# Kernel optimization log

Hardware: AMD Instinct MI355X
Metric: run time of the kernel (lower is better)

## Reference

```python
import jax, jax.numpy as jnp
import numpy as np

N_NODES = 100000
N_EDGES = 1600000
D = 128  # in_feats = n_hidden = out_feats


def _linear_params(key, d_in, d_out):
    kw, kb = jax.random.split(key)
    scale = 1.0 / np.sqrt(d_in)
    W = jax.random.uniform(kw, (d_in, d_out), jnp.float32, -scale, scale)
    b = jax.random.uniform(kb, (d_out,), jnp.float32, -scale, scale)
    return W, b


def setup_inputs() -> dict:
    key = jax.random.key(0)
    keys = jax.random.split(key, 8)
    x = jax.random.normal(keys[0], (N_NODES, D), jnp.float32)
    edge_index = jax.random.randint(keys[1], (2, N_EDGES), 0, N_NODES, jnp.int64)
    inp = {"x": x, "edge_index": edge_index}
    for l in range(3):
        W1, b1 = _linear_params(keys[2 + 2 * l], D, D)
        W2, b2 = _linear_params(keys[3 + 2 * l], D, D)
        inp[f"W1_{l}"] = W1
        inp[f"b1_{l}"] = b1
        inp[f"W2_{l}"] = W2
        inp[f"b2_{l}"] = b2
    return inp


def _gin_conv(x, src, dst, W1, b1, W2, b2):
    # GINConv: MLP((1+eps)*x + sum_{j->i} x_j), eps=0
    agg = jax.ops.segment_sum(x[src], dst, num_segments=N_NODES)
    h = agg + x
    h = jnp.maximum(h @ W1 + b1, 0.0)
    return h @ W2 + b2


def reference(x, edge_index, W1_0, b1_0, W2_0, b2_0,
              W1_1, b1_1, W2_1, b2_1, W1_2, b1_2, W2_2, b2_2):
    src, dst = edge_index[0], edge_index[1]
    # layer 0 (loop body): conv -> relu
    x = jnp.maximum(_gin_conv(x, src, dst, W1_0, b1_0, W2_0, b2_0), 0.0)
    # layer 1 (num_layers-2): conv -> relu -> dropout (eval: identity)
    x = jnp.maximum(_gin_conv(x, src, dst, W1_1, b1_1, W2_1, b2_1), 0.0)
    # layer 2 (last): conv -> relu
    x = jnp.maximum(_gin_conv(x, src, dst, W1_2, b1_2, W2_2, b2_2), 0.0)
    return x
```

## Files before the change

kernel.cpp:

```cpp
#include <hip/hip_runtime.h>

#define N_NODES 100000
#define N_EDGES 1600000
#define D 128
#define NBUCK 98
#define CAP 20480

typedef __attribute__((ext_vector_type(8))) short bf16x8;
typedef __attribute__((ext_vector_type(4))) float f32x4;
typedef unsigned long long u64;

__device__ __forceinline__ float b2f_lo(unsigned int u) {
    return __builtin_bit_cast(float, u << 16);
}
__device__ __forceinline__ float b2f_hi(unsigned int u) {
    return __builtin_bit_cast(float, u & 0xFFFF0000u);
}
__device__ __forceinline__ unsigned short f2b(float f) {
    unsigned int u = __builtin_bit_cast(unsigned int, f);
    u += 0x7FFFu + ((u >> 16) & 1u);
    return (unsigned short)(u >> 16);
}


__global__ __launch_bounds__(256) void prep_kernel(
    const float* __restrict__ x, unsigned short* __restrict__ xb,
    const float* __restrict__ W0, const float* __restrict__ W1_, const float* __restrict__ W2_,
    const float* __restrict__ W3, const float* __restrict__ W4, const float* __restrict__ W5,
    unsigned short* __restrict__ T0, unsigned short* __restrict__ T1_,
    unsigned short* __restrict__ T2_, unsigned short* __restrict__ T3,
    unsigned short* __restrict__ T4, unsigned short* __restrict__ T5,
    uint4* __restrict__ dob4, uint4* __restrict__ xbs4) {
    int blk = blockIdx.x;
    if (blk < 384) {
        const float* W;
        unsigned short* T;
        switch (blk >> 6) {
            case 0: W = W0; T = T0; break;
            case 1: W = W1_; T = T1_; break;
            case 2: W = W2_; T = T2_; break;
            case 3: W = W3; T = T3; break;
            case 4: W = W4; T = T4; break;
            default: W = W5; T = T5; break;
        }
        int i = (blk & 63) * 256 + threadIdx.x;
        int k = i >> 7, n = i & 127;
        T[n * 128 + k] = f2b(W[i]);
    } else if (blk < 12884) {
        int i = (blk - 384) * 256 + threadIdx.x;
        if (i < 3200000) {
            float4 v = ((const float4*)x)[i];
            ushort4 o;
            o.x = f2b(v.x); o.y = f2b(v.y); o.z = f2b(v.z); o.w = f2b(v.w);
            ((ushort4*)xb)[i] = o;
        }
    } else {
        int i = (blk - 12884) * 256 + threadIdx.x;
        uint4 z = {0u, 0u, 0u, 0u};
        if (i < 256) dob4[i] = z;
        if (i < 16) xbs4[i] = z;
    }
}


__global__ __launch_bounds__(256) void bin_kernel(const int* __restrict__ src,
                                                  const int* __restrict__ dst,
                                                  int* __restrict__ bcur,
                                                  u64* __restrict__ ebuf) {
    __shared__ int h[NBUCK];
    __shared__ int base[NBUCK];
    int tid = threadIdx.x;
    if (tid < NBUCK) h[tid] = 0;
    __syncthreads();
    int e0 = blockIdx.x * 2048;
    int myd[8], mys[8];
#pragma unroll
    for (int i = 0; i < 8; i++) {
        int e = e0 + tid + i * 256;
        int dv = (e < N_EDGES) ? dst[e] : -1;
        myd[i] = dv;
        mys[i] = (e < N_EDGES) ? src[e] : 0;
        if (dv >= 0) atomicAdd(&h[dv >> 10], 1);
    }
    __syncthreads();
    if (tid < NBUCK) {
        int c = h[tid];
        base[tid] = (c > 0) ? (tid * CAP + atomicAdd(&bcur[tid], c)) : 0;
        h[tid] = 0;
    }
    __syncthreads();
#pragma unroll
    for (int i = 0; i < 8; i++) {
        int dv = myd[i];
        if (dv >= 0) {
            int b = dv >> 10;
            int p = base[b] + atomicAdd(&h[b], 1);
            if (p < (b + 1) * CAP)
                ebuf[p] = ((u64)(unsigned int)dv << 32) | (unsigned int)mys[i];
        }
    }
}

__global__ __launch_bounds__(1024) void bucket_hist_kernel(const u64* __restrict__ ebuf,
                                                           const int* __restrict__ bcur,
                                                           int* __restrict__ deg,
                                                           int* __restrict__ ptot) {
    __shared__ int hist[1024];
    int b = blockIdx.x, tid = threadIdx.x;
    int nE = bcur[b]; if (nE > CAP) nE = CAP;
    const u64* slab = ebuf + (size_t)b * CAP;
    hist[tid] = 0;
    __syncthreads();
    for (int i = tid; i < nE; i += 1024)
        atomicAdd(&hist[(int)(slab[i] >> 32) & 1023], 1);
    __syncthreads();
    int node = b * 1024 + tid;
    int d = hist[tid];
    if (node < N_NODES) deg[node] = d;
    int dp = (node < N_NODES) ? ((d + 3) & ~3) : 0;
    __syncthreads();
    hist[tid] = dp;
    __syncthreads();
#pragma unroll
    for (int s = 512; s > 0; s >>= 1) {
        if (tid < s) hist[tid] += hist[tid + s];
        __syncthreads();
    }
    if (tid == 0) ptot[b] = hist[0];
}

__global__ __launch_bounds__(128) void pscan_kernel(const int* __restrict__ ptot,
                                                    int* __restrict__ bbase,
                                                    int* __restrict__ off) {
    __shared__ int s[128];
    int tid = threadIdx.x;
    int v = (tid < NBUCK) ? ptot[tid] : 0;
    s[tid] = v;
    __syncthreads();
#pragma unroll
    for (int d = 1; d < 128; d <<= 1) {
        int t = (tid >= d) ? s[tid - d] : 0;
        __syncthreads();
        s[tid] += t;
        __syncthreads();
    }
    if (tid < NBUCK) bbase[tid] = s[tid] - v;
    if (tid == 127) off[N_NODES] = s[127];
}

__global__ __launch_bounds__(1024) void bucket_csr_kernel(const u64* __restrict__ ebuf,
                                                          const int* __restrict__ bcur,
                                                          const int* __restrict__ deg,
                                                          const int* __restrict__ bbase,
                                                          int* __restrict__ off,
                                                          int* __restrict__ csr) {
    __shared__ int sc[1024];
    __shared__ int cnt[1024];
    int b = blockIdx.x, tid = threadIdx.x;
    int nE = bcur[b]; if (nE > CAP) nE = CAP;
    int base = bbase[b];
    const u64* slab = ebuf + (size_t)b * CAP;
    int node = b * 1024 + tid;
    int d = (node < N_NODES) ? deg[node] : 0;
    int dp = (node < N_NODES) ? ((d + 3) & ~3) : 0;
    sc[tid] = dp;
    cnt[tid] = 0;
    __syncthreads();
#pragma unroll
    for (int s = 1; s < 1024; s <<= 1) {
        int t = (tid >= s) ? sc[tid - s] : 0;
        __syncthreads();
        sc[tid] += t;
        __syncthreads();
    }
    int excl = sc[tid] - dp;
    sc[tid] = excl;
    if (node < N_NODES) off[node] = base + excl;
    __syncthreads();
    for (int i = tid; i < nE; i += 1024) {
        u64 e = slab[i];
        int dd = (int)(e >> 32) & 1023;
        int pos = sc[dd] + atomicAdd(&cnt[dd], 1);
        csr[base + pos] = (int)(e & 0xFFFFFFFFu);
    }
    for (int j = d; j < dp; j++) csr[base + excl + j] = N_NODES;
}


__global__ __launch_bounds__(256) void agg_bf16(const uint4* __restrict__ xb4,
                                                const int* __restrict__ off,
                                                const int* __restrict__ csr,
                                                uint4* __restrict__ t4) {
    int node = blockIdx.x * 4 + (threadIdx.x >> 6);
    if (node >= N_NODES) return;
    int lane = threadIdx.x & 63;
    int g = lane >> 4;
    int c = lane & 15;
    uint4 me = xb4[(size_t)node * 16 + c];
    float w0 = (g == 0) ? 1.0f : 0.0f;
    float a0 = b2f_lo(me.x) * w0, a1 = b2f_hi(me.x) * w0;
    float a2 = b2f_lo(me.y) * w0, a3 = b2f_hi(me.y) * w0;
    float a4 = b2f_lo(me.z) * w0, a5 = b2f_hi(me.z) * w0;
    float a6 = b2f_lo(me.w) * w0, a7 = b2f_hi(me.w) * w0;
    int k = off[node], e = off[node + 1];
#define PICK4(q) ((g & 2) ? ((g & 1) ? (q).w : (q).z) : ((g & 1) ? (q).y : (q).x))
#define ACC8(v) { a0 += b2f_lo((v).x); a1 += b2f_hi((v).x); \
                  a2 += b2f_lo((v).y); a3 += b2f_hi((v).y); \
                  a4 += b2f_lo((v).z); a5 += b2f_hi((v).z); \
                  a6 += b2f_lo((v).w); a7 += b2f_hi((v).w); }
    for (; k + 16 <= e; k += 16) {
        int4 q0 = *(const int4*)(csr + k);
        int4 q1 = *(const int4*)(csr + k + 4);
        int4 q2 = *(const int4*)(csr + k + 8);
        int4 q3 = *(const int4*)(csr + k + 12);
        int n0 = PICK4(q0), n1 = PICK4(q1), n2 = PICK4(q2), n3 = PICK4(q3);
        uint4 v0 = xb4[(size_t)n0 * 16 + c];
        uint4 v1 = xb4[(size_t)n1 * 16 + c];
        uint4 v2 = xb4[(size_t)n2 * 16 + c];
        uint4 v3 = xb4[(size_t)n3 * 16 + c];
        ACC8(v0); ACC8(v1); ACC8(v2); ACC8(v3);
    }
    for (; k < e; k += 4) {
        int4 q = *(const int4*)(csr + k);
        int n = PICK4(q);
        uint4 v = xb4[(size_t)n * 16 + c];
        ACC8(v);
    }
#undef PICK4
#undef ACC8
    a0 += __shfl_xor(a0, 16); a1 += __shfl_xor(a1, 16);
    a2 += __shfl_xor(a2, 16); a3 += __shfl_xor(a3, 16);
    a4 += __shfl_xor(a4, 16); a5 += __shfl_xor(a5, 16);
    a6 += __shfl_xor(a6, 16); a7 += __shfl_xor(a7, 16);
    a0 += __shfl_xor(a0, 32); a1 += __shfl_xor(a1, 32);
    a2 += __shfl_xor(a2, 32); a3 += __shfl_xor(a3, 32);
    a4 += __shfl_xor(a4, 32); a5 += __shfl_xor(a5, 32);
    a6 += __shfl_xor(a6, 32); a7 += __shfl_xor(a7, 32);
    if (g == 0) {
        uint4 o;
        o.x = (unsigned int)f2b(a0) | ((unsigned int)f2b(a1) << 16);
        o.y = (unsigned int)f2b(a2) | ((unsigned int)f2b(a3) << 16);
        o.z = (unsigned int)f2b(a4) | ((unsigned int)f2b(a5) << 16);
        o.w = (unsigned int)f2b(a6) | ((unsigned int)f2b(a7) << 16);
        t4[(size_t)node * 16 + c] = o;
    }
}


template <bool OUT_F32>
__global__ __launch_bounds__(256) void mlp_mfma(const unsigned short* __restrict__ A,
                                                const unsigned short* __restrict__ W1t,
                                                const float* __restrict__ bias1,
                                                const unsigned short* __restrict__ W2t,
                                                const float* __restrict__ bias2,
                                                void* __restrict__ out) {
    __shared__ char smem[4 * 8704];
    int tid = threadIdx.x;
    int wave = tid >> 6, lane = tid & 63;
    int quad = lane >> 4, mr = lane & 15;
    int m_base = blockIdx.x * 128 + wave * 32;
    int m0 = m_base + mr;       if (m0 >= N_NODES) m0 = N_NODES - 1;
    int m1 = m_base + 16 + mr;  if (m1 >= N_NODES) m1 = N_NODES - 1;

    unsigned short* ust = (unsigned short*)(smem + wave * 8704);

    bf16x8 a0[4], a1[4];
#pragma unroll
    for (int kc = 0; kc < 4; kc++) {
        a0[kc] = *(const bf16x8*)(A + (size_t)m0 * D + kc * 32 + quad * 8);
        a1[kc] = *(const bf16x8*)(A + (size_t)m1 * D + kc * 32 + quad * 8);
    }

    f32x4 acc0[8], acc1[8];
#pragma unroll
    for (int nt = 0; nt < 8; nt++) { acc0[nt] = (f32x4)0.0f; acc1[nt] = (f32x4)0.0f; }
#pragma unroll
    for (int nt = 0; nt < 8; nt++) {
        const unsigned short* wp = W1t + (size_t)(nt * 16 + mr) * D + quad * 8;
#pragma unroll
        for (int kc = 0; kc < 4; kc++) {
            bf16x8 b = *(const bf16x8*)(wp + kc * 32);
            acc0[nt] = __builtin_amdgcn_mfma_f32_16x16x32_bf16(a0[kc], b, acc0[nt], 0, 0, 0);
            acc1[nt] = __builtin_amdgcn_mfma_f32_16x16x32_bf16(a1[kc], b, acc1[nt], 0, 0, 0);
        }
    }
#pragma unroll
    for (int nt = 0; nt < 8; nt++) {
        float bv = bias1[nt * 16 + mr];
#pragma unroll
        for (int r = 0; r < 4; r++) {
            ust[(quad * 4 + r) * 136 + nt * 16 + mr] = f2b(fmaxf(acc0[nt][r] + bv, 0.0f));
            ust[2176 + (quad * 4 + r) * 136 + nt * 16 + mr] = f2b(fmaxf(acc1[nt][r] + bv, 0.0f));
        }
    }

#pragma unroll
    for (int kc = 0; kc < 4; kc++) {
        a0[kc] = *(const bf16x8*)&ust[mr * 136 + kc * 32 + quad * 8];
        a1[kc] = *(const bf16x8*)&ust[2176 + mr * 136 + kc * 32 + quad * 8];
    }
#pragma unroll
    for (int nt = 0; nt < 8; nt++) { acc0[nt] = (f32x4)0.0f; acc1[nt] = (f32x4)0.0f; }
#pragma unroll
    for (int nt = 0; nt < 8; nt++) {
        const unsigned short* wp = W2t + (size_t)(nt * 16 + mr) * D + quad * 8;
#pragma unroll
        for (int kc = 0; kc < 4; kc++) {
            bf16x8 b = *(const bf16x8*)(wp + kc * 32);
            acc0[nt] = __builtin_amdgcn_mfma_f32_16x16x32_bf16(a0[kc], b, acc0[nt], 0, 0, 0);
            acc1[nt] = __builtin_amdgcn_mfma_f32_16x16x32_bf16(a1[kc], b, acc1[nt], 0, 0, 0);
        }
    }

    if (OUT_F32) {
        float* st = (float*)ust;
        const int S = 132;
        float* op = (float*)out;
#pragma unroll
        for (int s = 0; s < 2; s++) {
#pragma unroll
            for (int nt = 0; nt < 8; nt++) {
                float bv = bias2[nt * 16 + mr];
#pragma unroll
                for (int r = 0; r < 4; r++) {
                    float v = s ? acc1[nt][r] : acc0[nt][r];
                    st[(quad * 4 + r) * S + nt * 16 + mr] = fmaxf(v + bv, 0.0f);
                }
            }
#pragma unroll
            for (int it = 0; it < 8; it++) {
                int linear = lane + it * 64;
                int row = linear >> 5, col = (linear & 31) << 2;
                int gm = m_base + s * 16 + row;
                if (gm < N_NODES) {
                    float4 val = *(float4*)&st[row * S + col];
                    *(float4*)(op + (size_t)gm * D + col) = val;
                }
            }
        }
    } else {
        const int S = 136;
        unsigned short* op = (unsigned short*)out;
#pragma unroll
        for (int s = 0; s < 2; s++) {
            unsigned short* st = ust + s * 2176;
#pragma unroll
            for (int nt = 0; nt < 8; nt++) {
                float bv = bias2[nt * 16 + mr];
#pragma unroll
                for (int r = 0; r < 4; r++) {
                    float v = s ? acc1[nt][r] : acc0[nt][r];
                    st[(quad * 4 + r) * S + nt * 16 + mr] = f2b(fmaxf(v + bv, 0.0f));
                }
            }
#pragma unroll
            for (int it = 0; it < 4; it++) {
                int linear = lane + it * 64;
                int row = linear >> 4, col = (linear & 15) << 3;
                int gm = m_base + s * 16 + row;
                if (gm < N_NODES) {
                    uint4 val = *(uint4*)&st[row * S + col];
                    *(uint4*)(op + (size_t)gm * D + col) = val;
                }
            }
        }
    }
}


extern "C" void kernel_launch(void* const* d_in, const int* in_sizes, int n_in,
                              void* d_out, int out_size, void* d_ws, size_t ws_size,
                              hipStream_t stream) {
    const float* x = (const float*)d_in[0];
    const int* ei = (const int*)d_in[1];
    const int* srcv = ei;
    const int* dstv = ei + N_EDGES;
    const float* W1[3] = {(const float*)d_in[2], (const float*)d_in[6], (const float*)d_in[10]};
    const float* b1[3] = {(const float*)d_in[3], (const float*)d_in[7], (const float*)d_in[11]};
    const float* W2[3] = {(const float*)d_in[4], (const float*)d_in[8], (const float*)d_in[12]};
    const float* b2[3] = {(const float*)d_in[5], (const float*)d_in[9], (const float*)d_in[13]};

    char* ws = (char*)d_ws;
    int* off = (int*)ws;
    unsigned short* Wt[6];
    for (int i = 0; i < 6; i++) Wt[i] = (unsigned short*)(ws + 401408 + i * 32768);
    int* csr = (int*)(ws + 598016);
    unsigned short* xb = (unsigned short*)(ws + 8198144);
    unsigned short* P  = (unsigned short*)(ws + 33798400);

    char* dob = (char*)d_out;
    int* bcur  = (int*)(dob);
    int* deg   = (int*)(dob + 4096);
    int* ptot  = (int*)(dob + 450560);
    int* bbase = (int*)(dob + 454656);
    u64* ebuf  = (u64*)(dob + 1048576);

    prep_kernel<<<12885, 256, 0, stream>>>(
        x, xb,
        W1[0], W2[0], W1[1], W2[1], W1[2], W2[2],
        Wt[0], Wt[1], Wt[2], Wt[3], Wt[4], Wt[5],
        (uint4*)dob, (uint4*)(xb + (size_t)N_NODES * D));

    bin_kernel<<<782, 256, 0, stream>>>(srcv, dstv, bcur, ebuf);
    bucket_hist_kernel<<<NBUCK, 1024, 0, stream>>>(ebuf, bcur, deg, ptot);
    pscan_kernel<<<1, 128, 0, stream>>>(ptot, bbase, off);
    bucket_csr_kernel<<<NBUCK, 1024, 0, stream>>>(ebuf, bcur, deg, bbase, off, csr);

    const int agg_grid = 25000;
    const int mlp_grid = (N_NODES + 127) / 128;

    agg_bf16<<<agg_grid, 256, 0, stream>>>((const uint4*)xb, off, csr, (uint4*)P);
    mlp_mfma<false><<<mlp_grid, 256, 0, stream>>>(P, Wt[0], b1[0], Wt[1], b2[0], xb);
    agg_bf16<<<agg_grid, 256, 0, stream>>>((const uint4*)xb, off, csr, (uint4*)P);
    mlp_mfma<false><<<mlp_grid, 256, 0, stream>>>(P, Wt[2], b1[1], Wt[3], b2[1], xb);
    agg_bf16<<<agg_grid, 256, 0, stream>>>((const uint4*)xb, off, csr, (uint4*)P);
    mlp_mfma<true><<<mlp_grid, 256, 0, stream>>>(P, Wt[4], b1[2], Wt[5], b2[2], d_out);
}
```

Baseline: 504.9 us.

## Split bf16 features into 8 column-group planes for cache-resident gather aggregation

Stores node features as 8 column-group planes of 16 bf16 values each (32 bytes per node per plane). The aggregation kernel gives each block a single column group, so the gathered working set per plane (~3.2 MB) can stay in cache, with 8 lanes per node and edge indices shuffled across lanes. CSR padding goes from multiples of 4 to multiples of 8, and the CSR array moves into the output buffer. The MLP loads and stores are adapted to the planar layout, at the cost of 32-byte gather granularity and more padded edges.

```diff
diff --git a/kernel.cpp b/kernel.cpp
--- a/kernel.cpp
+++ b/kernel.cpp
@@ -5,6 +5,8 @@
 #define D 128
 #define NBUCK 98
 #define CAP 20480
+#define RSTRIDE_U32 800008
+#define RSTRIDE_S 1600016
 
 typedef __attribute__((ext_vector_type(8))) short bf16x8;
 typedef __attribute__((ext_vector_type(4))) float f32x4;
@@ -24,13 +26,13 @@
 
 
 __global__ __launch_bounds__(256) void prep_kernel(
-    const float* __restrict__ x, unsigned short* __restrict__ xb,
+    const float* __restrict__ x, unsigned int* __restrict__ xbT,
     const float* __restrict__ W0, const float* __restrict__ W1_, const float* __restrict__ W2_,
     const float* __restrict__ W3, const float* __restrict__ W4, const float* __restrict__ W5,
     unsigned short* __restrict__ T0, unsigned short* __restrict__ T1_,
     unsigned short* __restrict__ T2_, unsigned short* __restrict__ T3,
     unsigned short* __restrict__ T4, unsigned short* __restrict__ T5,
-    uint4* __restrict__ dob4, uint4* __restrict__ xbs4) {
+    uint4* __restrict__ dob4) {
     int blk = blockIdx.x;
     if (blk < 384) {
         const float* W;
@@ -50,15 +52,24 @@
         int i = (blk - 384) * 256 + threadIdx.x;
         if (i < 3200000) {
             float4 v = ((const float4*)x)[i];
-            ushort4 o;
-            o.x = f2b(v.x); o.y = f2b(v.y); o.z = f2b(v.z); o.w = f2b(v.w);
-            ((ushort4*)xb)[i] = o;
+            int r = i >> 5;
+            int q = i & 31;
+            int dw = q * 2;
+            int cg = dw >> 3;
+            int cj = dw & 7;
+            uint2 o;
+            o.x = (unsigned int)f2b(v.x) | ((unsigned int)f2b(v.y) << 16);
+            o.y = (unsigned int)f2b(v.z) | ((unsigned int)f2b(v.w) << 16);
+            *(uint2*)(xbT + (size_t)cg * RSTRIDE_U32 + (size_t)r * 8 + cj) = o;
         }
     } else {
         int i = (blk - 12884) * 256 + threadIdx.x;
         uint4 z = {0u, 0u, 0u, 0u};
         if (i < 256) dob4[i] = z;
-        if (i < 16) xbs4[i] = z;
+        if (i < 64) {
+            int cg = i >> 3, c = i & 7;
+            xbT[(size_t)cg * RSTRIDE_U32 + (size_t)N_NODES * 8 + c] = 0u;
+        }
     }
 }
 
@@ -117,7 +128,7 @@
     int node = b * 1024 + tid;
     int d = hist[tid];
     if (node < N_NODES) deg[node] = d;
-    int dp = (node < N_NODES) ? ((d + 3) & ~3) : 0;
+    int dp = (node < N_NODES) ? ((d + 7) & ~7) : 0;
     __syncthreads();
     hist[tid] = dp;
     __syncthreads();
@@ -162,7 +173,7 @@
     const u64* slab = ebuf + (size_t)b * CAP;
     int node = b * 1024 + tid;
     int d = (node < N_NODES) ? deg[node] : 0;
-    int dp = (node < N_NODES) ? ((d + 3) & ~3) : 0;
+    int dp = (node < N_NODES) ? ((d + 7) & ~7) : 0;
     sc[tid] = dp;
     cnt[tid] = 0;
     __syncthreads();
@@ -187,63 +198,32 @@
 }
 
 
-__global__ __launch_bounds__(256) void agg_bf16(const uint4* __restrict__ xb4,
-                                                const int* __restrict__ off,
-                                                const int* __restrict__ csr,
-                                                uint4* __restrict__ t4) {
-    int node = blockIdx.x * 4 + (threadIdx.x >> 6);
-    if (node >= N_NODES) return;
+__global__ __launch_bounds__(256) void agg_cg(const unsigned int* __restrict__ xbT,
+                                              const int* __restrict__ off,
+                                              const int* __restrict__ csr,
+                                              unsigned int* __restrict__ tT) {
+    int cg = blockIdx.x & 7;
+    int nb = blockIdx.x >> 3;
     int lane = threadIdx.x & 63;
-    int g = lane >> 4;
-    int c = lane & 15;
-    uint4 me = xb4[(size_t)node * 16 + c];
-    float w0 = (g == 0) ? 1.0f : 0.0f;
-    float a0 = b2f_lo(me.x) * w0, a1 = b2f_hi(me.x) * w0;
-    float a2 = b2f_lo(me.y) * w0, a3 = b2f_hi(me.y) * w0;
-    float a4 = b2f_lo(me.z) * w0, a5 = b2f_hi(me.z) * w0;
-    float a6 = b2f_lo(me.w) * w0, a7 = b2f_hi(me.w) * w0;
+    int wave = threadIdx.x >> 6;
+    int grp = lane >> 3, c = lane & 7;
+    const unsigned int* xr = xbT + (size_t)cg * RSTRIDE_U32;
+    unsigned int* tr = tT + (size_t)cg * RSTRIDE_U32;
+    int node = nb * 32 + wave * 8 + grp;
     int k = off[node], e = off[node + 1];
-#define PICK4(q) ((g & 2) ? ((g & 1) ? (q).w : (q).z) : ((g & 1) ? (q).y : (q).x))
-#define ACC8(v) { a0 += b2f_lo((v).x); a1 += b2f_hi((v).x); \
-                  a2 += b2f_lo((v).y); a3 += b2f_hi((v).y); \
-                  a4 += b2f_lo((v).z); a5 += b2f_hi((v).z); \
-                  a6 += b2f_lo((v).w); a7 += b2f_hi((v).w); }
-    for (; k + 16 <= e; k += 16) {
-        int4 q0 = *(const int4*)(csr + k);
-        int4 q1 = *(const int4*)(csr + k + 4);
-        int4 q2 = *(const int4*)(csr + k + 8);
-        int4 q3 = *(const int4*)(csr + k + 12);
-        int n0 = PICK4(q0), n1 = PICK4(q1), n2 = PICK4(q2), n3 = PICK4(q3);
-        uint4 v0 = xb4[(size_t)n0 * 16 + c];
-        uint4 v1 = xb4[(size_t)n1 * 16 + c];
-        uint4 v2 = xb4[(size_t)n2 * 16 + c];
-        uint4 v3 = xb4[(size_t)n3 * 16 + c];
-        ACC8(v0); ACC8(v1); ACC8(v2); ACC8(v3);
-    }
-    for (; k < e; k += 4) {
-        int4 q = *(const int4*)(csr + k);
-        int n = PICK4(q);
-        uint4 v = xb4[(size_t)n * 16 + c];
-        ACC8(v);
-    }
-#undef PICK4
-#undef ACC8
-    a0 += __shfl_xor(a0, 16); a1 += __shfl_xor(a1, 16);
-    a2 += __shfl_xor(a2, 16); a3 += __shfl_xor(a3, 16);
-    a4 += __shfl_xor(a4, 16); a5 += __shfl_xor(a5, 16);
-    a6 += __shfl_xor(a6, 16); a7 += __shfl_xor(a7, 16);
-    a0 += __shfl_xor(a0, 32); a1 += __shfl_xor(a1, 32);
-    a2 += __shfl_xor(a2, 32); a3 += __shfl_xor(a3, 32);
-    a4 += __shfl_xor(a4, 32); a5 += __shfl_xor(a5, 32);
-    a6 += __shfl_xor(a6, 32); a7 += __shfl_xor(a7, 32);
-    if (g == 0) {
-        uint4 o;
-        o.x = (unsigned int)f2b(a0) | ((unsigned int)f2b(a1) << 16);
-        o.y = (unsigned int)f2b(a2) | ((unsigned int)f2b(a3) << 16);
-        o.z = (unsigned int)f2b(a4) | ((unsigned int)f2b(a5) << 16);
-        o.w = (unsigned int)f2b(a6) | ((unsigned int)f2b(a7) << 16);
-        t4[(size_t)node * 16 + c] = o;
-    }
+    unsigned int me = xr[(size_t)node * 8 + c];
+    float alo = b2f_lo(me), ahi = b2f_hi(me);
+    for (; k < e; k += 8) {
+        int idx = csr[k + c];
+#pragma unroll
+        for (int i = 0; i < 8; i++) {
+            int n = __shfl(idx, i, 8);
+            unsigned int v = xr[(size_t)n * 8 + c];
+            alo += b2f_lo(v);
+            ahi += b2f_hi(v);
+        }
+    }
+    tr[(size_t)node * 8 + c] = (unsigned int)f2b(alo) | ((unsigned int)f2b(ahi) << 16);
 }
 
 
@@ -267,8 +247,9 @@
     bf16x8 a0[4], a1[4];
 #pragma unroll
     for (int kc = 0; kc < 4; kc++) {
-        a0[kc] = *(const bf16x8*)(A + (size_t)m0 * D + kc * 32 + quad * 8);
-        a1[kc] = *(const bf16x8*)(A + (size_t)m1 * D + kc * 32 + quad * 8);
+        size_t rb = (size_t)(2 * kc + (quad >> 1)) * RSTRIDE_S + (size_t)((quad & 1) * 8);
+        a0[kc] = *(const bf16x8*)(A + rb + (size_t)m0 * 16);
+        a1[kc] = *(const bf16x8*)(A + rb + (size_t)m1 * 16);
     }
 
     f32x4 acc0[8], acc1[8];
@@ -356,11 +337,13 @@
 #pragma unroll
             for (int it = 0; it < 4; it++) {
                 int linear = lane + it * 64;
-                int row = linear >> 4, col = (linear & 15) << 3;
+                int row = linear >> 4, colst = (linear & 15) << 3;
                 int gm = m_base + s * 16 + row;
                 if (gm < N_NODES) {
-                    uint4 val = *(uint4*)&st[row * S + col];
-                    *(uint4*)(op + (size_t)gm * D + col) = val;
+                    uint4 val = *(uint4*)&st[row * S + colst];
+                    unsigned short* dp = op + (size_t)(colst >> 4) * RSTRIDE_S
+                                       + (size_t)gm * 16 + (colst & 15);
+                    *(uint4*)dp = val;
                 }
             }
         }
@@ -384,9 +367,8 @@
     int* off = (int*)ws;
     unsigned short* Wt[6];
     for (int i = 0; i < 6; i++) Wt[i] = (unsigned short*)(ws + 401408 + i * 32768);
-    int* csr = (int*)(ws + 598016);
-    unsigned short* xb = (unsigned short*)(ws + 8198144);
-    unsigned short* P  = (unsigned short*)(ws + 33798400);
+    unsigned short* xbT = (unsigned short*)(ws + 598016);
+    unsigned short* PT  = (unsigned short*)(ws + 26198272);
 
     char* dob = (char*)d_out;
     int* bcur  = (int*)(dob);
@@ -394,12 +376,13 @@
     int* ptot  = (int*)(dob + 450560);
     int* bbase = (int*)(dob + 454656);
     u64* ebuf  = (u64*)(dob + 1048576);
+    int* csr   = (int*)(dob + 17104896);
 
     prep_kernel<<<12885, 256, 0, stream>>>(
-        x, xb,
+        x, (unsigned int*)xbT,
         W1[0], W2[0], W1[1], W2[1], W1[2], W2[2],
         Wt[0], Wt[1], Wt[2], Wt[3], Wt[4], Wt[5],
-        (uint4*)dob, (uint4*)(xb + (size_t)N_NODES * D));
+        (uint4*)dob);
 
     bin_kernel<<<782, 256, 0, stream>>>(srcv, dstv, bcur, ebuf);
     bucket_hist_kernel<<<NBUCK, 1024, 0, stream>>>(ebuf, bcur, deg, ptot);
@@ -409,10 +392,10 @@
     const int agg_grid = 25000;
     const int mlp_grid = (N_NODES + 127) / 128;
 
-    agg_bf16<<<agg_grid, 256, 0, stream>>>((const uint4*)xb, off, csr, (uint4*)P);
-    mlp_mfma<false><<<mlp_grid, 256, 0, stream>>>(P, Wt[0], b1[0], Wt[1], b2[0], xb);
-    agg_bf16<<<agg_grid, 256, 0, stream>>>((const uint4*)xb, off, csr, (uint4*)P);
-    mlp_mfma<false><<<mlp_grid, 256, 0, stream>>>(P, Wt[2], b1[1], Wt[3], b2[1], xb);
-    agg_bf16<<<agg_grid, 256, 0, stream>>>((const uint4*)xb, off, csr, (uint4*)P);
-    mlp_mfma<true><<<mlp_grid, 256, 0, stream>>>(P, Wt[4], b1[2], Wt[5], b2[2], d_out);
-}
+    agg_cg<<<agg_grid, 256, 0, stream>>>((const unsigned int*)xbT, off, csr, (unsigned int*)PT);
+    mlp_mfma<false><<<mlp_grid, 256, 0, stream>>>(PT, Wt[0], b1[0], Wt[1], b2[0], xbT);
+    agg_cg<<<agg_grid, 256, 0, stream>>>((const unsigned int*)xbT, off, csr, (unsigned int*)PT);
+    mlp_mfma<false><<<mlp_grid, 256, 0, stream>>>(PT, Wt[2], b1[1], Wt[3], b2[1], xbT);
+    agg_cg<<<agg_grid, 256, 0, stream>>>((const unsigned int*)xbT, off, csr, (unsigned int*)PT);
+    mlp_mfma<true><<<mlp_grid, 256, 0, stream>>>(PT, Wt[4], b1[2], Wt[5], b2[2], d_out);
+}
```

Result: slower. 524.0 us (+3.8%).

## Fuse neighbor aggregation into MLP kernel with ping-pong feature buffers

Applied to the files above, without the earlier changes.

Replaces the separate aggregation and MLP kernels with one per-layer kernel. Each 64-thread block aggregates 32 nodes into shared memory, then runs the MFMA MLP on them directly, so the aggregated intermediate never goes through global memory. Two feature buffers alternate between layers so a layer never overwrites its own input. In exchange, each block is a single wave that loops over its 32 nodes serially, with 4-byte gathers and lower memory-level parallelism than the old 4-waves-per-block gather. The shared-memory indexing for the second 16-row tile also looks questionable.

```diff
diff --git a/kernel.cpp b/kernel.cpp
--- a/kernel.cpp
+++ b/kernel.cpp
@@ -30,7 +30,7 @@
     unsigned short* __restrict__ T0, unsigned short* __restrict__ T1_,
     unsigned short* __restrict__ T2_, unsigned short* __restrict__ T3,
     unsigned short* __restrict__ T4, unsigned short* __restrict__ T5,
-    uint4* __restrict__ dob4, uint4* __restrict__ xbs4) {
+    uint4* __restrict__ dob4, uint4* __restrict__ xs0, uint4* __restrict__ xs1) {
     int blk = blockIdx.x;
     if (blk < 384) {
         const float* W;
@@ -58,7 +58,7 @@
         int i = (blk - 12884) * 256 + threadIdx.x;
         uint4 z = {0u, 0u, 0u, 0u};
         if (i < 256) dob4[i] = z;
-        if (i < 16) xbs4[i] = z;
+        if (i < 16) { xs0[i] = z; xs1[i] = z; }
     }
 }
 
@@ -187,88 +187,60 @@
 }
 
 
-__global__ __launch_bounds__(256) void agg_bf16(const uint4* __restrict__ xb4,
-                                                const int* __restrict__ off,
-                                                const int* __restrict__ csr,
-                                                uint4* __restrict__ t4) {
-    int node = blockIdx.x * 4 + (threadIdx.x >> 6);
-    if (node >= N_NODES) return;
-    int lane = threadIdx.x & 63;
-    int g = lane >> 4;
-    int c = lane & 15;
-    uint4 me = xb4[(size_t)node * 16 + c];
-    float w0 = (g == 0) ? 1.0f : 0.0f;
-    float a0 = b2f_lo(me.x) * w0, a1 = b2f_hi(me.x) * w0;
-    float a2 = b2f_lo(me.y) * w0, a3 = b2f_hi(me.y) * w0;
-    float a4 = b2f_lo(me.z) * w0, a5 = b2f_hi(me.z) * w0;
-    float a6 = b2f_lo(me.w) * w0, a7 = b2f_hi(me.w) * w0;
-    int k = off[node], e = off[node + 1];
-#define PICK4(q) ((g & 2) ? ((g & 1) ? (q).w : (q).z) : ((g & 1) ? (q).y : (q).x))
-#define ACC8(v) { a0 += b2f_lo((v).x); a1 += b2f_hi((v).x); \
-                  a2 += b2f_lo((v).y); a3 += b2f_hi((v).y); \
-                  a4 += b2f_lo((v).z); a5 += b2f_hi((v).z); \
-                  a6 += b2f_lo((v).w); a7 += b2f_hi((v).w); }
-    for (; k + 16 <= e; k += 16) {
-        int4 q0 = *(const int4*)(csr + k);
-        int4 q1 = *(const int4*)(csr + k + 4);
-        int4 q2 = *(const int4*)(csr + k + 8);
-        int4 q3 = *(const int4*)(csr + k + 12);
-        int n0 = PICK4(q0), n1 = PICK4(q1), n2 = PICK4(q2), n3 = PICK4(q3);
-        uint4 v0 = xb4[(size_t)n0 * 16 + c];
-        uint4 v1 = xb4[(size_t)n1 * 16 + c];
-        uint4 v2 = xb4[(size_t)n2 * 16 + c];
-        uint4 v3 = xb4[(size_t)n3 * 16 + c];
-        ACC8(v0); ACC8(v1); ACC8(v2); ACC8(v3);
-    }
-    for (; k < e; k += 4) {
-        int4 q = *(const int4*)(csr + k);
-        int n = PICK4(q);
-        uint4 v = xb4[(size_t)n * 16 + c];
-        ACC8(v);
-    }
-#undef PICK4
-#undef ACC8
-    a0 += __shfl_xor(a0, 16); a1 += __shfl_xor(a1, 16);
-    a2 += __shfl_xor(a2, 16); a3 += __shfl_xor(a3, 16);
-    a4 += __shfl_xor(a4, 16); a5 += __shfl_xor(a5, 16);
-    a6 += __shfl_xor(a6, 16); a7 += __shfl_xor(a7, 16);
-    a0 += __shfl_xor(a0, 32); a1 += __shfl_xor(a1, 32);
-    a2 += __shfl_xor(a2, 32); a3 += __shfl_xor(a3, 32);
-    a4 += __shfl_xor(a4, 32); a5 += __shfl_xor(a5, 32);
-    a6 += __shfl_xor(a6, 32); a7 += __shfl_xor(a7, 32);
-    if (g == 0) {
-        uint4 o;
-        o.x = (unsigned int)f2b(a0) | ((unsigned int)f2b(a1) << 16);
-        o.y = (unsigned int)f2b(a2) | ((unsigned int)f2b(a3) << 16);
-        o.z = (unsigned int)f2b(a4) | ((unsigned int)f2b(a5) << 16);
-        o.w = (unsigned int)f2b(a6) | ((unsigned int)f2b(a7) << 16);
-        t4[(size_t)node * 16 + c] = o;
-    }
-}
-
-
 template <bool OUT_F32>
-__global__ __launch_bounds__(256) void mlp_mfma(const unsigned short* __restrict__ A,
-                                                const unsigned short* __restrict__ W1t,
-                                                const float* __restrict__ bias1,
-                                                const unsigned short* __restrict__ W2t,
-                                                const float* __restrict__ bias2,
-                                                void* __restrict__ out) {
-    __shared__ char smem[4 * 8704];
-    int tid = threadIdx.x;
-    int wave = tid >> 6, lane = tid & 63;
+__global__ __launch_bounds__(64, 3) void gin_layer(const unsigned int* __restrict__ xbu,
+                                                   const int* __restrict__ off,
+                                                   const int* __restrict__ csr,
+                                                   const unsigned short* __restrict__ W1t,
+                                                   const float* __restrict__ bias1,
+                                                   const unsigned short* __restrict__ W2t,
+                                                   const float* __restrict__ bias2,
+                                                   void* __restrict__ out) {
+    __shared__ unsigned int smem[2176];
+    int lane = threadIdx.x;
     int quad = lane >> 4, mr = lane & 15;
-    int m_base = blockIdx.x * 128 + wave * 32;
-    int m0 = m_base + mr;       if (m0 >= N_NODES) m0 = N_NODES - 1;
-    int m1 = m_base + 16 + mr;  if (m1 >= N_NODES) m1 = N_NODES - 1;
-
-    unsigned short* ust = (unsigned short*)(smem + wave * 8704);
+    int m_base = blockIdx.x * 32;
+
+    for (int s = 0; s < 32; s++) {
+        int node = m_base + s;
+        unsigned int me = xbu[(size_t)node * 64 + lane];
+        float ax = b2f_lo(me), ay = b2f_hi(me);
+        int k = off[node], e = off[node + 1];
+        for (; k + 8 <= e; k += 8) {
+            int n0 = csr[k + 0], n1 = csr[k + 1], n2 = csr[k + 2], n3 = csr[k + 3];
+            int n4 = csr[k + 4], n5 = csr[k + 5], n6 = csr[k + 6], n7 = csr[k + 7];
+            unsigned int g0 = xbu[(size_t)n0 * 64 + lane];
+            unsigned int g1 = xbu[(size_t)n1 * 64 + lane];
+            unsigned int g2 = xbu[(size_t)n2 * 64 + lane];
+            unsigned int g3 = xbu[(size_t)n3 * 64 + lane];
+            unsigned int g4 = xbu[(size_t)n4 * 64 + lane];
+            unsigned int g5 = xbu[(size_t)n5 * 64 + lane];
+            unsigned int g6 = xbu[(size_t)n6 * 64 + lane];
+            unsigned int g7 = xbu[(size_t)n7 * 64 + lane];
+            ax += b2f_lo(g0) + b2f_lo(g1) + b2f_lo(g2) + b2f_lo(g3)
+                + b2f_lo(g4) + b2f_lo(g5) + b2f_lo(g6) + b2f_lo(g7);
+            ay += b2f_hi(g0) + b2f_hi(g1) + b2f_hi(g2) + b2f_hi(g3)
+                + b2f_hi(g4) + b2f_hi(g5) + b2f_hi(g6) + b2f_hi(g7);
+        }
+        if (k < e) {
+            int n0 = csr[k + 0], n1 = csr[k + 1], n2 = csr[k + 2], n3 = csr[k + 3];
+            unsigned int g0 = xbu[(size_t)n0 * 64 + lane];
+            unsigned int g1 = xbu[(size_t)n1 * 64 + lane];
+            unsigned int g2 = xbu[(size_t)n2 * 64 + lane];
+            unsigned int g3 = xbu[(size_t)n3 * 64 + lane];
+            ax += b2f_lo(g0) + b2f_lo(g1) + b2f_lo(g2) + b2f_lo(g3);
+            ay += b2f_hi(g0) + b2f_hi(g1) + b2f_hi(g2) + b2f_hi(g3);
+        }
+        smem[s * 68 + lane] = (unsigned int)f2b(ax) | ((unsigned int)f2b(ay) << 16);
+    }
+
+    unsigned short* ust = (unsigned short*)smem;
 
     bf16x8 a0[4], a1[4];
 #pragma unroll
     for (int kc = 0; kc < 4; kc++) {
-        a0[kc] = *(const bf16x8*)(A + (size_t)m0 * D + kc * 32 + quad * 8);
-        a1[kc] = *(const bf16x8*)(A + (size_t)m1 * D + kc * 32 + quad * 8);
+        a0[kc] = *(const bf16x8*)&ust[mr * 136 + kc * 32 + quad * 8];
+        a1[kc] = *(const bf16x8*)&ust[2176 + mr * 136 + kc * 32 + quad * 8];
     }
 
     f32x4 acc0[8], acc1[8];
@@ -313,7 +285,7 @@
     }
 
     if (OUT_F32) {
-        float* st = (float*)ust;
+        float* st = (float*)smem;
         const int S = 132;
         float* op = (float*)out;
 #pragma unroll
@@ -383,10 +355,10 @@
     char* ws = (char*)d_ws;
     int* off = (int*)ws;
     unsigned short* Wt[6];
-    for (int i = 0; i < 6; i++) Wt[i] = (unsigned short*)(ws + 401408 + i * 32768);
-    int* csr = (int*)(ws + 598016);
-    unsigned short* xb = (unsigned short*)(ws + 8198144);
-    unsigned short* P  = (unsigned short*)(ws + 33798400);
+    for (int i = 0; i < 6; i++) Wt[i] = (unsigned short*)(ws + 400016 + i * 32768);
+    unsigned short* xb0 = (unsigned short*)(ws + 596624);
+    unsigned short* xb1 = (unsigned short*)(ws + 26196880);
+    int* csr = (int*)(ws + 51797136);
 
     char* dob = (char*)d_out;
     int* bcur  = (int*)(dob);
@@ -396,23 +368,24 @@
     u64* ebuf  = (u64*)(dob + 1048576);
 
     prep_kernel<<<12885, 256, 0, stream>>>(
-        x, xb,
+        x, xb0,
         W1[0], W2[0], W1[1], W2[1], W1[2], W2[2],
         Wt[0], Wt[1], Wt[2], Wt[3], Wt[4], Wt[5],
-        (uint4*)dob, (uint4*)(xb + (size_t)N_NODES * D));
+        (uint4*)dob,
+        (uint4*)(xb0 + (size_t)N_NODES * D),
+        (uint4*)(xb1 + (size_t)N_NODES * D));
 
     bin_kernel<<<782, 256, 0, stream>>>(srcv, dstv, bcur, ebuf);
     bucket_hist_kernel<<<NBUCK, 1024, 0, stream>>>(ebuf, bcur, deg, ptot);
     pscan_kernel<<<1, 128, 0, stream>>>(ptot, bbase, off);
     bucket_csr_kernel<<<NBUCK, 1024, 0, stream>>>(ebuf, bcur, deg, bbase, off, csr);
 
-    const int agg_grid = 25000;
-    const int mlp_grid = (N_NODES + 127) / 128;
-
-    agg_bf16<<<agg_grid, 256, 0, stream>>>((const uint4*)xb, off, csr, (uint4*)P);
-    mlp_mfma<false><<<mlp_grid, 256, 0, stream>>>(P, Wt[0], b1[0], Wt[1], b2[0], xb);
-    agg_bf16<<<agg_grid, 256, 0, stream>>>((const uint4*)xb, off, csr, (uint4*)P);
-    mlp_mfma<false><<<mlp_grid, 256, 0, stream>>>(P, Wt[2], b1[1], Wt[3], b2[1], xb);
-    agg_bf16<<<agg_grid, 256, 0, stream>>>((const uint4*)xb, off, csr, (uint4*)P);
-    mlp_mfma<true><<<mlp_grid, 256, 0, stream>>>(P, Wt[4], b1[2], Wt[5], b2[2], d_out);
-}
+    const int grid = N_NODES / 32;
+
+    gin_layer<false><<<grid, 64, 0, stream>>>((const unsigned int*)xb0, off, csr,
+                                              Wt[0], b1[0], Wt[1], b2[0], xb1);
+    gin_layer<false><<<grid, 64, 0, stream>>>((const unsigned int*)xb1, off, csr,
+                                              Wt[2], b1[1], Wt[3], b2[1], xb0);
+    gin_layer<true><<<grid, 64, 0, stream>>>((const unsigned int*)xb0, off, csr,
+                                             Wt[4], b1[2], Wt[5], b2[2], d_out);
+}
```

Measured after the change: 620.2 us. 1.23x slower.
